# Optimization experiments

Measured on AMD Instinct MI355X. Metric: run time of the kernel, lower is better.

Reference implementation:

```python
import jax, jax.numpy as jnp
import numpy as np

N, E, G = 51200, 819200, 256            # nodes, directed edges, graphs
N2, A, E2 = 102400, 204800, 409600      # 2-sets, assignments, 2-set edges
D, L, NI2, NAF = 64, 5, 36, 40          # emb_dim, num_layer, num_i_2, num_atom_features
EPS = 1e-5


def _seg_sum(v, seg, n):
    return jax.ops.segment_sum(v, seg, num_segments=n)


def _seg_mean(v, seg, n):
    s = jax.ops.segment_sum(v, seg, num_segments=n)
    c = jax.ops.segment_sum(jnp.ones((v.shape[0],), v.dtype), seg, num_segments=n)
    return s / jnp.maximum(c, 1.0)[:, None]


def setup_inputs() -> dict:
    key = jax.random.key(0)
    ks = iter(jax.random.split(key, 64))
    nrm = lambda shape: jax.random.normal(next(ks), shape, jnp.float32) * 0.1
    x = jax.random.normal(next(ks), (N, NAF), jnp.float32)
    edge_index = jax.random.randint(next(ks), (2, E), 0, N, dtype=jnp.int32)
    edge_attr = jnp.stack([jax.random.randint(next(ks), (E,), 0, 4, dtype=jnp.int32),
                           jax.random.randint(next(ks), (E,), 0, 3, dtype=jnp.int32)], axis=1)
    batch = jnp.repeat(jnp.arange(G, dtype=jnp.int32), N // G)
    iso_type_2 = jax.nn.one_hot(jax.random.randint(next(ks), (N2,), 0, NI2), NI2, dtype=jnp.float32)
    edge_index_2 = jax.random.randint(next(ks), (2, E2), 0, N2, dtype=jnp.int32)
    assignment_index_2 = jnp.stack([jax.random.randint(next(ks), (A,), 0, N, dtype=jnp.int32),
                                    jnp.repeat(jnp.arange(N2, dtype=jnp.int32), 2)], axis=0)
    batch_2 = jnp.repeat(jnp.arange(G, dtype=jnp.int32), N2 // G)
    params = dict(
        emb_W=nrm((NAF, D)), emb_b=jnp.zeros((D,), jnp.float32),
        gin_W1=nrm((L, D, 2 * D)), gin_b1=jnp.zeros((L, 2 * D), jnp.float32),
        gin_W2=nrm((L, 2 * D, D)), gin_b2=jnp.zeros((L, D), jnp.float32),
        eemb1=nrm((L, 6, D)), eemb2=nrm((L, 3, D)),
        bn_gamma=jnp.ones((L, D), jnp.float32), bn_beta=jnp.zeros((L, D), jnp.float32),
        iso1_rel_W=nrm((D + NI2, D)), iso1_rel_b=jnp.zeros((D,), jnp.float32),
        iso1_root_W=nrm((D + NI2, D)),
        iso2_rel_W=nrm((D, D)), iso2_rel_b=jnp.zeros((D,), jnp.float32),
        iso2_root_W=nrm((D, D)),
        ro_W0=nrm((2 * D, D)), ro_b0=jnp.zeros((D,), jnp.float32),
        ro_W1=nrm((D, D // 2)), ro_b1=jnp.zeros((D // 2,), jnp.float32),
        ro_W2=nrm((D // 2, D // 4)), ro_b2=jnp.zeros((D // 4,), jnp.float32),
        last_W=nrm((D // 4, 1)), last_b=jnp.zeros((1,), jnp.float32),
    )
    return dict(x=x, edge_index=edge_index, edge_attr=edge_attr, batch=batch,
                iso_type_2=iso_type_2, edge_index_2=edge_index_2,
                assignment_index_2=assignment_index_2, batch_2=batch_2, **params)


def _forward(x, iso_type_2, emb_W, emb_b, gin_W1, gin_b1, gin_W2, gin_b2,
             eemb1, eemb2, bn_gamma, bn_beta,
             iso1_rel_W, iso1_rel_b, iso1_root_W, iso2_rel_W, iso2_rel_b, iso2_root_W,
             ro_W0, ro_b0, ro_W1, ro_b1, ro_W2, ro_b2, last_W, last_b,
             edge_index, edge_attr, batch, edge_index_2, assignment_index_2, batch_2):
    # --- GIN stack with edge-feature embeddings and self loops ---
    loop = jnp.arange(N, dtype=edge_index.dtype)
    src = jnp.concatenate([edge_index[0], loop])
    dst = jnp.concatenate([edge_index[1], loop])
    sl_attr = jnp.tile(jnp.array([[4, 0]], dtype=edge_attr.dtype), (N, 1))
    ea = jnp.concatenate([edge_attr, sl_attr], axis=0)  # [E+N, 2]

    h = jax.nn.relu(x @ emb_W + emb_b)  # x_embedding1
    for l in range(L):
        e = eemb1[l][ea[:, 0]] + eemb2[l][ea[:, 1]]      # [E+N, D]
        agg = _seg_sum(h[src] + e, dst, N)               # gather + scatter-add
        h2 = jax.nn.relu(agg @ gin_W1[l] + gin_b1[l]) @ gin_W2[l] + gin_b2[l]
        mu = jnp.mean(h2, axis=0)
        var = jnp.var(h2, axis=0)                        # biased, torch BN training mode
        h2 = (h2 - mu) / jnp.sqrt(var + EPS) * bn_gamma[l] + bn_beta[l]
        h = h2 if l == L - 1 else jax.nn.relu(h2)        # last layer: no ReLU (JK='last')
    node_rep = h

    # --- graph mean pool of node representation ---
    x1 = _seg_mean(node_rep, batch, G)                   # [G, D]

    # --- 2-set branch: avg_pool onto 2-sets, concat iso type, two GraphConvs ---
    xp = _seg_mean(node_rep[assignment_index_2[0]], assignment_index_2[1], N2)
    xp = jnp.concatenate([xp, iso_type_2], axis=1)       # [N2, D+NI2]

    def graph_conv(z, Wrel, brel, Wroot):
        agg = _seg_sum(z[edge_index_2[0]], edge_index_2[1], N2)
        return agg @ Wrel + brel + z @ Wroot

    xp = jax.nn.relu(graph_conv(xp, iso1_rel_W, iso1_rel_b, iso1_root_W))
    xp = jax.nn.relu(graph_conv(xp, iso2_rel_W, iso2_rel_b, iso2_root_W))
    x2 = _seg_mean(xp, batch_2, G)                       # [G, D]

    # --- readout MLP ---
    m = jnp.concatenate([x1, x2], axis=1)                # [G, 2D]
    m = jax.nn.relu(m @ ro_W0 + ro_b0)
    m = jax.nn.relu(m @ ro_W1 + ro_b1)
    m = jax.nn.relu(m @ ro_W2 + ro_b2)
    m = m @ last_W + last_b
    return m.reshape(-1)                                 # num_tasks == 1 -> flat [G]


def reference(x, edge_index, edge_attr, batch, iso_type_2, edge_index_2,
              assignment_index_2, batch_2, emb_W, emb_b, gin_W1, gin_b1, gin_W2,
              gin_b2, eemb1, eemb2, bn_gamma, bn_beta, iso1_rel_W, iso1_rel_b,
              iso1_root_W, iso2_rel_W, iso2_rel_b, iso2_root_W, ro_W0, ro_b0,
              ro_W1, ro_b1, ro_W2, ro_b2, last_W, last_b):
    return _forward(x, iso_type_2, emb_W, emb_b, gin_W1, gin_b1, gin_W2, gin_b2,
                    eemb1, eemb2, bn_gamma, bn_beta,
                    iso1_rel_W, iso1_rel_b, iso1_root_W, iso2_rel_W, iso2_rel_b,
                    iso2_root_W, ro_W0, ro_b0, ro_W1, ro_b1, ro_W2, ro_b2,
                    last_W, last_b, edge_index, edge_attr, batch, edge_index_2,
                    assignment_index_2, batch_2)
```

## Files before the change

kernel.cpp:

```cpp
#include <hip/hip_runtime.h>

#define NN   51200
#define EE   819200
#define GG   256
#define NN2  102400
#define AA   204800
#define EE2  409600
#define DD   64
#define LL   5

#define NB1  100
#define NB2  200
#define CAP1 10240
#define CAP2 3072

typedef __attribute__((ext_vector_type(8))) short bf16x8;
typedef __attribute__((ext_vector_type(4))) float f32x4;
typedef unsigned short ushort_t;

#define OFF_H      ((size_t)0)
#define OFF_AGG    ((size_t)13107200)
#define OFF_H2     ((size_t)26214400)
#define OFF_XP     ((size_t)39321600)
#define OFF_REC1   OFF_XP
// ... 110 lines not shown
    int v = (tid < nb) ? cnt[tid] : 0;
    int incl = waveInclScan(v, lane);
    if (lane == 63) wsum[wid] = incl;
    __syncthreads();
    int woff = 0;
#pragma unroll
    for (int w = 0; w < 3; ++w) woff += (w < wid) ? wsum[w] : 0;
    if (tid < nb) base[tid] = woff + incl - v;
}

__global__ __launch_bounds__(256) void kbB(const int* __restrict__ bucketCnt,
                                           const int* __restrict__ bucketBase,
                                           const int2* __restrict__ rec1, const int2* __restrict__ rec2,
                                           int* __restrict__ offs1, int* __restrict__ col1,
                                           int* __restrict__ offs2, int* __restrict__ col2,
                                           int* __restrict__ dbin) {
    __shared__ int nh[512];
    __shared__ int ncur[512];
    __shared__ int wsum[4];
    __shared__ int dhist[64];
    int tid = threadIdx.x, b = blockIdx.x;
    bool g1 = b < NB1;
    const int2* rec = g1 ? (rec1 + (size_t)b * CAP1) : (rec2 + (size_t)(b - NB1) * CAP2);
    int cnt = bucketCnt[b];
    int base = bucketBase[b];
    int* offs = g1 ? offs1 : offs2;
    int* col = g1 ? col1 : col2;
    int nodeBase = g1 ? b * 512 : (b - NB1) * 512;
    nh[tid] = 0; nh[tid + 256] = 0;
    if (tid < 64) dhist[tid] = 0;
    __syncthreads();
    for (int e = tid; e < cnt; e += 256) {
        int2 r = rec[e];
        atomicAdd(&nh[r.y & 511], 1);
    }
    __syncthreads();
    int v0 = nh[2 * tid], v1 = nh[2 * tid + 1];
    int s = v0 + v1;
    int lane = tid & 63, wid = tid >> 6;
    int incl = waveInclScan(s, lane);
    if (lane == 63) wsum[wid] = incl;
    __syncthreads();
    int woff = 0;
#pragma unroll
    for (int w = 0; w < 3; ++w) woff += (w < wid) ? wsum[w] : 0;
    int excl = woff + incl - s;
    ncur[2 * tid] = excl;
    ncur[2 * tid + 1] = excl + v0;
    offs[nodeBase + 2 * tid] = base + excl;
    offs[nodeBase + 2 * tid + 1] = base + excl + v0;
    if (g1) {
        atomicAdd(&dhist[v0 < 63 ? v0 : 63], 1);
        atomicAdd(&dhist[v1 < 63 ? v1 : 63], 1);
    }
    __syncthreads();
    for (int e = tid; e < cnt; e += 256) {
        int2 r = rec[e];
        int node = r.y & 511;
        int slot = base + atomicAdd(&ncur[node], 1);
        col[slot] = r.x;
    }
    if (g1 && tid < 64 && dhist[tid]) atomicAdd(&dbin[tid], dhist[tid]);
    if (tid == 0) {
        if (b == NB1 - 1) offs1[NN] = EE;
        if (b == NB1 + NB2 - 1) offs2[NN2] = EE2;
    }
}

__global__ __launch_bounds__(256) void kiso(const float* __restrict__ iso, int* __restrict__ isoIdx) {
    __shared__ float srow[256 * 36];
    int tid = threadIdx.x;
    int base = blockIdx.x * 256;
    const float4* g4p = (const float4*)(iso + (size_t)base * 36);
#pragma unroll
    for (int i = tid; i < 2304; i += 256) ((float4*)srow)[i] = g4p[i];
    __syncthreads();
    const float* r = srow + tid * 36;
    int best = 0;
#pragma unroll
    for (int k = 0; k < 36; ++k)
        if (r[k] > 0.5f) best = k;
    isoIdx[base + tid] = best;
}

__global__ void kprepx(const float* __restrict__ x, const float* __restrict__ embW,
                       const float* __restrict__ embB, float* __restrict__ h,
                       const float* __restrict__ gW1, const float* __restrict__ gW2,
                       ushort_t* __restrict__ w1h, ushort_t* __restrict__ w1l,
                       ushort_t* __restrict__ w2h, ushort_t* __restrict__ w2l,
                       const float* __restrict__ i1rW, const float* __restrict__ i1tW,
                       const float* __restrict__ i2rW, const float* __restrict__ i2tW,
                       ushort_t* __restrict__ gcwh, ushort_t* __restrict__ gcwl) {
    int b = blockIdx.x;
    if (b < 12800) {
        int t = b * 256 + threadIdx.x;
        int n = t >> 6, d = t & 63;
        float acc = embB[d];
        const float4* xr4 = (const float4*)(x + (size_t)n * 40);
#pragma unroll
        for (int k4 = 0; k4 < 10; ++k4) {
            float4 xv = xr4[k4];
            acc = fmaf(xv.x, embW[(4 * k4 + 0) * 64 + d], acc);
            acc = fmaf(xv.y, embW[(4 * k4 + 1) * 64 + d], acc);
            acc = fmaf(xv.z, embW[(4 * k4 + 2) * 64 + d], acc);
            acc = fmaf(xv.w, embW[(4 * k4 + 3) * 64 + d], acc);
        }
        h[(size_t)n * 64 + d] = fmaxf(acc, 0.f);
    } else if (b < 12840) {
        int t = (b - 12800) * 256 + threadIdx.x;
        int lane = t & 63, frag = t >> 6;
        int c15 = lane & 15, q = lane >> 4;
        if (frag < 80) {
            int kt = frag & 1, nt = (frag >> 1) & 7, l = frag >> 4;
            const float* W = gW1 + l * 8192;
            ushort_t* oh = w1h + ((size_t)frag * 64 + lane) * 8;
            ushort_t* ol = w1l + ((size_t)frag * 64 + lane) * 8;
            int kb = kt * 32 + q * 8, colw = nt * 16 + c15;
#pragma unroll
            for (int j = 0; j < 8; ++j) {
                ushort_t hi, lo; bsplit(W[(kb + j) * 128 + colw], hi, lo);
                oh[j] = hi; ol[j] = lo;
            }
        } else if (frag < 160) {
            int f = frag - 80;
            int kt = f & 3, nt = (f >> 2) & 3, l = f >> 4;
            const float* W = gW2 + l * 8192;
            ushort_t* oh = w2h + ((size_t)f * 64 + lane) * 8;
            ushort_t* ol = w2l + ((size_t)f * 64 + lane) * 8;
            int kb = kt * 32 + q * 8, colw = nt * 16 + c15;
#pragma unroll
            for (int j = 0; j < 8; ++j) {
                ushort_t hi, lo; bsplit(W[(kb + j) * 64 + colw], hi, lo);
                oh[j] = hi; ol[j] = lo;
            }
        }
    } else {
        int t = (b - 12840) * 256 + threadIdx.x;
        int lane = t & 63, frag = t >> 6;
        int c15 = lane & 15, q = lane >> 4;
        int m = frag >> 3, f = frag & 7;
        int kt = f & 1, nt = f >> 1;
        const float* W = (m == 0) ? i1rW : (m == 1) ? i1tW : (m == 2) ? i2rW : i2tW;
        ushort_t* oh = gcwh + (size_t)m * 4096 + ((size_t)f * 64 + lane) * 8;
        ushort_t* ol = gcwl + (size_t)m * 4096 + ((size_t)f * 64 + lane) * 8;
        int kb = kt * 32 + q * 8, colw = nt * 16 + c15;
#pragma unroll
        for (int j = 0; j < 8; ++j) {
            ushort_t hi, lo; bsplit(W[(kb + j) * 64 + colw], hi, lo);
            oh[j] = hi; ol[j] = lo;
        }
    }
}

__global__ void kdegscan(const int* __restrict__ dbin, int* __restrict__ dstart) {
    int tid = threadIdx.x;
    int v = dbin[tid];
    int incl = waveInclScan(v, tid);
    dstart[tid] = incl - v;
}

__global__ __launch_bounds__(256) void kdegplace(const int* __restrict__ offs,
                                                 const int* __restrict__ dstart,
                                                 int* __restrict__ dcur,
                                                 int* __restrict__ perm) {
    __shared__ int lhist[64];
    __shared__ int lbase[64];
    int tid = threadIdx.x;
    if (tid < 64) lhist[tid] = 0;
    __syncthreads();
    int n = blockIdx.x * 256 + tid;
    int d = offs[n + 1] - offs[n]; d = d < 63 ? d : 63;
    int lr = atomicAdd(&lhist[d], 1);
    __syncthreads();
    if (tid < 64) {
        int c = lhist[tid];
        lbase[tid] = c ? atomicAdd(&dcur[tid], c) : 0;
    }
    __syncthreads();
    perm[dstart[d] + lbase[d] + lr] = n;
}

__global__ __launch_bounds__(256) void ktrans(float* __restrict__ h,
                                              const float* __restrict__ pst,
                                              const float* __restrict__ gamma,
                                              const float* __restrict__ beta) {
    __shared__ float sstat[128];
    __shared__ float sSC[64], sSH[64];
    int tid = threadIdx.x;
    if (tid < 128) {
        float s = 0.f;
        const float* p = pst + tid;
#pragma unroll
        for (int i = 0; i < 32; ++i) s += p[i * 128];
        sstat[tid] = s;
    }
    __syncthreads();
    if (tid < 64) {
        float mu = sstat[tid] * (1.f / NN);
        float var = sstat[64 + tid] * (1.f / NN) - mu * mu;
        float sc = gamma[tid] * rsqrtf(var + 1e-5f);
        sSC[tid] = sc; sSH[tid] = beta[tid] - mu * sc;
    }
    __syncthreads();
    int c = (tid & 15) * 4;
    float4 sc4 = *(const float4*)(sSC + c);
    float4 sh4 = *(const float4*)(sSH + c);
    float4* hp = (float4*)h;
    size_t base = (size_t)blockIdx.x * 1024 + tid;
#pragma unroll
    for (int r = 0; r < 4; ++r) {
        float4 v = hp[base + r * 256];
        v.x = fmaxf(fmaf(v.x, sc4.x, sh4.x), 0.f);
        v.y = fmaxf(fmaf(v.y, sc4.y, sh4.y), 0.f);
        v.z = fmaxf(fmaf(v.z, sc4.z, sh4.z), 0.f);
        v.w = fmaxf(fmaf(v.w, sc4.w, sh4.w), 0.f);
        hp[base + r * 256] = v;
    }
}

__global__ __launch_bounds__(256) void kglayer(
    const float* __restrict__ hin, float* __restrict__ hout,
    const int* __restrict__ perm,
    const int* __restrict__ offs, const int* __restrict__ col,
    const float* __restrict__ e1, const float* __restrict__ e2,
    const ushort_t* __restrict__ w1h, const ushort_t* __restrict__ w1l,
    const ushort_t* __restrict__ w2h, const ushort_t* __restrict__ w2l,
    const float* __restrict__ b1, const float* __restrict__ b2,
    float* __restrict__ pstout) {
    __shared__ float etab[13 * 64];
    __shared__ int sPerm[16];
    __shared__ float sMLP[16 * 132];
    float* sA = sMLP;
    float* sH = sMLP;
    int tid = threadIdx.x;
    if (tid < 16) sPerm[tid] = perm[blockIdx.x * 16 + tid];
    for (int idx = tid; idx < 13 * 64; idx += 256) {
        int ci = idx >> 6, dd = idx & 63;
        etab[idx] = e1[(ci / 3) * 64 + dd] + e2[(ci % 3) * 64 + dd];
    }
    __syncthreads();
    int lane = tid & 63, wv = tid >> 6;
    int c15 = lane & 15, q = lane >> 4;

    {
        int n = sPerm[wv * 4 + q];
        int s0 = offs[n], s1 = offs[n + 1];
        float4 sx = *(const float4*)(hin + (size_t)n * 64 + 4 * c15);
        float4 et = *(const float4*)(etab + 12 * 64 + 4 * c15);
        float a0 = sx.x + et.x, a1 = sx.y + et.y, a2 = sx.z + et.z, a3 = sx.w + et.w;
        int deg = s1 - s0;
        if (deg > 0) {
            const int* cp = col + s0;
            int nfull = deg >> 3, rem = deg & 7;
            int vv[8];
#pragma unroll
            for (int j = 0; j < 8; ++j) {
                int idx = j < deg ? j : deg - 1;
                vv[j] = cp[idx];
            }
            for (int it = 0; it < nfull; ++it) {
                float4 xv[8], tv[8];
#pragma unroll
                for (int j = 0; j < 8; ++j) {
                    xv[j] = *(const float4*)(hin + (size_t)(vv[j] & 0xFFFF) * 64 + 4 * c15);
                    tv[j] = *(const float4*)(etab + (vv[j] >> 16) * 64 + 4 * c15);
                }
                int e8 = (it + 1) * 8;
                bool more = e8 < deg;
                int nx[8];
                if (more) {
#pragma unroll
                    for (int j = 0; j < 8; ++j) {
                        int idx = e8 + j; idx = idx < deg ? idx : deg - 1;
                        nx[j] = cp[idx];
                    }
                }
#pragma unroll
                for (int j = 0; j < 8; ++j) {
                    a0 += xv[j].x + tv[j].x;
                    a1 += xv[j].y + tv[j].y;
                    a2 += xv[j].z + tv[j].z;
                    a3 += xv[j].w + tv[j].w;
                }
                if (more) {
#pragma unroll
                    for (int j = 0; j < 8; ++j) vv[j] = nx[j];
                }
            }
            if (rem) {
                float4 xv[8], tv[8];
#pragma unroll
                for (int j = 0; j < 8; ++j) {
                    xv[j] = *(const float4*)(hin + (size_t)(vv[j] & 0xFFFF) * 64 + 4 * c15);
                    tv[j] = *(const float4*)(etab + (vv[j] >> 16) * 64 + 4 * c15);
                }
#pragma unroll
                for (int j = 0; j < 8; ++j) {
                    float mm = (j < rem) ? 1.f : 0.f;
                    a0 = fmaf(xv[j].x + tv[j].x, mm, a0);
                    a1 = fmaf(xv[j].y + tv[j].y, mm, a1);
                    a2 = fmaf(xv[j].z + tv[j].z, mm, a2);
                    a3 = fmaf(xv[j].w + tv[j].w, mm, a3);
                }
            }
        }
        *(float4*)(sA + (wv * 4 + q) * 68 + 4 * c15) = make_float4(a0, a1, a2, a3);
    }
    __syncthreads();

    bf16x8 ah[2], al[2];
#pragma unroll
    for (int kt = 0; kt < 2; ++kt) {
        const float* p = sA + c15 * 68 + kt * 32 + q * 8;
        float4 x0 = *(const float4*)p;
        float4 x1 = *(const float4*)(p + 4);
        float xs[8] = {x0.x, x0.y, x0.z, x0.w, x1.x, x1.y, x1.z, x1.w};
#pragma unroll
        for (int j = 0; j < 8; ++j) {
            ushort_t hi, lo; bsplit(xs[j], hi, lo);
            ah[kt][j] = (short)hi; al[kt][j] = (short)lo;
        }
    }
    __syncthreads();

    f32x4 acc1[2];
#pragma unroll
    for (int j = 0; j < 2; ++j) { f32x4 z = {0.f, 0.f, 0.f, 0.f}; acc1[j] = z; }
#pragma unroll
    for (int kt = 0; kt < 2; ++kt) {
#pragma unroll
        for (int j = 0; j < 2; ++j) {
            int nt = 2 * wv + j;
            size_t fo = ((size_t)((nt * 2 + kt) * 64 + lane)) * 8;
            bf16x8 bh = *(const bf16x8*)(w1h + fo);
            bf16x8 bl = *(const bf16x8*)(w1l + fo);
            acc1[j] = __builtin_amdgcn_mfma_f32_16x16x32_bf16(ah[kt], bh, acc1[j], 0, 0, 0);
            acc1[j] = __builtin_amdgcn_mfma_f32_16x16x32_bf16(al[kt], bh, acc1[j], 0, 0, 0);
            acc1[j] = __builtin_amdgcn_mfma_f32_16x16x32_bf16(ah[kt], bl, acc1[j], 0, 0, 0);
        }
    }
#pragma unroll
    for (int j = 0; j < 2; ++j) {
        int nt = 2 * wv + j;
        float bias = b1[nt * 16 + c15];
#pragma unroll
        for (int rg = 0; rg < 4; ++rg)
            sH[(4 * q + rg) * 132 + nt * 16 + c15] = fmaxf(acc1[j][rg] + bias, 0.f);
    }
    __syncthreads();

    f32x4 acc2 = {0.f, 0.f, 0.f, 0.f};
#pragma unroll
    for (int kt = 0; kt < 4; ++kt) {
        const float* p = sH + c15 * 132 + kt * 32 + q * 8;
        float4 x0 = *(const float4*)p;
        float4 x1 = *(const float4*)(p + 4);
        float xs[8] = {x0.x, x0.y, x0.z, x0.w, x1.x, x1.y, x1.z, x1.w};
        bf16x8 a2h, a2l;
#pragma unroll
        for (int j = 0; j < 8; ++j) {
            ushort_t hi, lo; bsplit(xs[j], hi, lo);
            a2h[j] = (short)hi; a2l[j] = (short)lo;
        }
        size_t fo = ((size_t)((wv * 4 + kt) * 64 + lane)) * 8;
        bf16x8 bh = *(const bf16x8*)(w2h + fo);
        bf16x8 bl = *(const bf16x8*)(w2l + fo);
        acc2 = __builtin_amdgcn_mfma_f32_16x16x32_bf16(a2h, bh, acc2, 0, 0, 0);
        acc2 = __builtin_amdgcn_mfma_f32_16x16x32_bf16(a2l, bh, acc2, 0, 0, 0);
        acc2 = __builtin_amdgcn_mfma_f32_16x16x32_bf16(a2h, bl, acc2, 0, 0, 0);
    }
    {
        float bias = b2[wv * 16 + c15];
        float s = 0.f, s2 = 0.f;
#pragma unroll
        for (int rg = 0; rg < 4; ++rg) {
            float v = acc2[rg] + bias;
            hout[(size_t)sPerm[4 * q + rg] * 64 + wv * 16 + c15] = v;
            s += v; s2 += v * v;
        }
        s += __shfl_xor(s, 16, 64);  s += __shfl_xor(s, 32, 64);
        s2 += __shfl_xor(s2, 16, 64); s2 += __shfl_xor(s2, 32, 64);
        if (q == 0) {
            float* ps = pstout + (size_t)(blockIdx.x & 31) * 128;
            atomicAdd(&ps[wv * 16 + c15], s);
            atomicAdd(&ps[64 + wv * 16 + c15], s2);
        }
    }
}

template <int FIRST>
__global__ __launch_bounds__(256) void kgcmm(const float* __restrict__ X,
                                             const ushort_t* __restrict__ grh,
                                             const ushort_t* __restrict__ grl,
                                             const ushort_t* __restrict__ gth,
                                             const ushort_t* __restrict__ gtl,
                                             const float* __restrict__ WrelIso,
                                             const float* __restrict__ WrootIso,
                                             const int* __restrict__ isoIdx,
                                             float* __restrict__ Yrel,
                                             float* __restrict__ Yroot,
                                             const float* __restrict__ pst,
                                             const float* __restrict__ g4,
                                             const float* __restrict__ b4,
                                             const int* __restrict__ a0g,
                                             const float* __restrict__ h2src) {
    __shared__ float sX[64 * 68];
    __shared__ float sstat[128];
    __shared__ float sSC[64], sSH[64];
    int tid = threadIdx.x, blk = blockIdx.x;
    if (FIRST && tid < 128) {
        float s = 0.f;
        const float* p = pst + tid;
#pragma unroll
        for (int i = 0; i < 32; ++i) s += p[i * 128];
        sstat[tid] = s;
    }
    __syncthreads();
    if (FIRST && tid < 64) {
        float mu = sstat[tid] * (1.f / NN);
        float var = sstat[64 + tid] * (1.f / NN) - mu * mu;
        float sc = g4[tid] * rsqrtf(var + 1e-5f);
        sSC[tid] = sc;
        sSH[tid] = b4[tid] - mu * sc;
    }
    __syncthreads();
#pragma unroll
    for (int i = tid; i < 1024; i += 256) {
        int row = i >> 4, c = (i & 15) << 2;
        float4 v;
        if (FIRST) {
            int grow = blk * 64 + row;
            int na = a0g[2 * grow], nb = a0g[2 * grow + 1];
            float4 va = *(const float4*)(h2src + (size_t)na * 64 + c);
            float4 vb = *(const float4*)(h2src + (size_t)nb * 64 + c);
            v.x = 0.5f * (va.x + vb.x); v.y = 0.5f * (va.y + vb.y);
            v.z = 0.5f * (va.z + vb.z); v.w = 0.5f * (va.w + vb.w);
            v.x = fmaf(v.x, sSC[c], sSH[c]);
            v.y = fmaf(v.y, sSC[c + 1], sSH[c + 1]);
            v.z = fmaf(v.z, sSC[c + 2], sSH[c + 2]);
            v.w = fmaf(v.w, sSC[c + 3], sSH[c + 3]);
        } else {
            v = ((const float4*)(X + (size_t)blk * 4096))[i];
        }
        float* p = sX + row * 68 + c;
        p[0] = v.x; p[1] = v.y; p[2] = v.z; p[3] = v.w;
    }
    __syncthreads();
    int lane = tid & 63, wv = tid >> 6;
    int c15 = lane & 15, q = lane >> 4;

    bf16x8 ah[2], al[2];
#pragma unroll
    for (int kt = 0; kt < 2; ++kt) {
        const float* p = sX + (16 * wv + c15) * 68 + kt * 32 + q * 8;
        float4 x0 = *(const float4*)p;
        float4 x1 = *(const float4*)(p + 4);
        float xs[8] = {x0.x, x0.y, x0.z, x0.w, x1.x, x1.y, x1.z, x1.w};
#pragma unroll
        for (int j = 0; j < 8; ++j) {
            ushort_t hi, lo; bsplit(xs[j], hi, lo);
            ah[kt][j] = (short)hi; al[kt][j] = (short)lo;
        }
    }

    f32x4 accR[4], accT[4];
#pragma unroll
    for (int nt = 0; nt < 4; ++nt) {
        f32x4 z = {0.f, 0.f, 0.f, 0.f};
        accR[nt] = z; accT[nt] = z;
    }
#pragma unroll
    for (int nt = 0; nt < 4; ++nt) {
#pragma unroll
        for (int kt = 0; kt < 2; ++kt) {
            size_t fo = ((size_t)((nt * 2 + kt) * 64 + lane)) * 8;
            bf16x8 bh = *(const bf16x8*)(grh + fo);
            bf16x8 bl = *(const bf16x8*)(grl + fo);
            accR[nt] = __builtin_amdgcn_mfma_f32_16x16x32_bf16(ah[kt], bh, accR[nt], 0, 0, 0);
            accR[nt] = __builtin_amdgcn_mfma_f32_16x16x32_bf16(al[kt], bh, accR[nt], 0, 0, 0);
            accR[nt] = __builtin_amdgcn_mfma_f32_16x16x32_bf16(ah[kt], bl, accR[nt], 0, 0, 0);
            bf16x8 ch = *(const bf16x8*)(gth + fo);
            bf16x8 cl = *(const bf16x8*)(gtl + fo);
            accT[nt] = __builtin_amdgcn_mfma_f32_16x16x32_bf16(ah[kt], ch, accT[nt], 0, 0, 0);
            accT[nt] = __builtin_amdgcn_mfma_f32_16x16x32_bf16(al[kt], ch, accT[nt], 0, 0, 0);
            accT[nt] = __builtin_amdgcn_mfma_f32_16x16x32_bf16(ah[kt], cl, accT[nt], 0, 0, 0);
        }
    }

    int rbase = blk * 64 + 16 * wv + 4 * q;
#pragma unroll
    for (int rg = 0; rg < 4; ++rg) {
        int row = rbase + rg;
        int ii = FIRST ? isoIdx[row] : 0;
        float* yr = Yrel + (size_t)row * 64;
        float* yt = Yroot + (size_t)row * 64;
        const float* er = WrelIso + (size_t)ii * 64;
        const float* et = WrootIso + (size_t)ii * 64;
#pragma unroll
        for (int nt = 0; nt < 4; ++nt) {
            int cc = nt * 16 + c15;
            float vr = accR[nt][rg], vt = accT[nt][rg];
            if (FIRST) { vr += er[cc]; vt += et[cc]; }
            yr[cc] = vr;
            yt[cc] = vt;
        }
    }
}

__global__ void kgather2(const float* __restrict__ yrel, const float* __restrict__ yroot,
                         const float* __restrict__ brel, const int* __restrict__ offs,
                         const int* __restrict__ col, float* __restrict__ out) {
    int t = blockIdx.x * 256 + threadIdx.x;
    int j = t >> 4, c = t & 15;
    int s0 = offs[j], s1 = offs[j + 1];
    float4 rt = *(const float4*)(yroot + (size_t)j * 64 + 4 * c);
    float4 bb = *(const float4*)(brel + 4 * c);
    float a0 = rt.x + bb.x, a1 = rt.y + bb.y, a2 = rt.z + bb.z, a3 = rt.w + bb.w;
    if (s0 < s1) {
        int vv[4];
#pragma unroll
        for (int jj = 0; jj < 4; ++jj) {
            int idx = s0 + jj; idx = idx < s1 ? idx : s1 - 1;
            vv[jj] = col[idx];
        }
        int e = s0;
        while (true) {
            int ne = e + 4;
            bool more = ne < s1;
            float4 xs[4];
#pragma unroll
            for (int jj = 0; jj < 4; ++jj)
                xs[jj] = *(const float4*)(yrel + (size_t)vv[jj] * 64 + 4 * c);
            int nx[4];
            if (more) {
#pragma unroll
                for (int jj = 0; jj < 4; ++jj) {
                    int idx = ne + jj; idx = idx < s1 ? idx : s1 - 1;
                    nx[jj] = col[idx];
                }
            }
#pragma unroll
            for (int jj = 0; jj < 4; ++jj) {
                float mm = (e + jj < s1) ? 1.f : 0.f;
                a0 = fmaf(xs[jj].x, mm, a0);
                a1 = fmaf(xs[jj].y, mm, a1);
                a2 = fmaf(xs[jj].z, mm, a2);
                a3 = fmaf(xs[jj].w, mm, a3);
            }
            if (!more) break;
            e = ne;
#pragma unroll
            for (int jj = 0; jj < 4; ++jj) vv[jj] = nx[jj];
        }
    }
    *(float4*)(out + (size_t)j * 64 + 4 * c) =
        make_float4(fmaxf(a0, 0.f), fmaxf(a1, 0.f), fmaxf(a2, 0.f), fmaxf(a3, 0.f));
}

__global__ void kpoolg(const float* __restrict__ h2, const float* __restrict__ xp2,
                       const float* __restrict__ pst, const float* __restrict__ g4,
                       const float* __restrict__ b4, float* __restrict__ m) {
    __shared__ float sstat[128];
    __shared__ float red[4][64];
    int g = blockIdx.x, tid = threadIdx.x;
    if (tid < 128) {
        float s = 0.f;
        const float* p = pst + tid;
#pragma unroll
        for (int i = 0; i < 32; ++i) s += p[i * 128];
        sstat[tid] = s;
    }
    int wid = tid >> 6, d = tid & 63;
    float s1 = 0.f;
    for (int i = wid; i < 200; i += 4) s1 += h2[((size_t)g * 200 + i) * 64 + d];
    red[wid][d] = s1;
    __syncthreads();
    if (wid == 0) {
        float mean = (red[0][d] + red[1][d] + red[2][d] + red[3][d]) * (1.f / 200.f);
        float mu = sstat[d] * (1.f / NN);
        float var = sstat[64 + d] * (1.f / NN) - mu * mu;
        float sc = g4[d] * rsqrtf(var + 1e-5f);
        m[g * 128 + d] = fmaf(mean, sc, b4[d] - mu * sc);
    }
    __syncthreads();
    float s2 = 0.f;
    for (int i = wid; i < 400; i += 4) s2 += xp2[((size_t)g * 400 + i) * 64 + d];
    red[wid][d] = s2;
    __syncthreads();
    if (wid == 0) m[g * 128 + 64 + d] = (red[0][d] + red[1][d] + red[2][d] + red[3][d]) * (1.f / 400.f);
}

__global__ void kread(const float* __restrict__ m, const float* __restrict__ W0,
                      const float* __restrict__ b0, const float* __restrict__ W1,
                      const float* __restrict__ b1, const float* __restrict__ W2,
                      const float* __restrict__ b2, const float* __restrict__ lw,
                      const float* __restrict__ lb, float* __restrict__ out) {
    __shared__ float s0[64], s1[32], s2[16];
    int g = blockIdx.x, d = threadIdx.x;
    const float* mr = m + g * 128;
    float t = b0[d];
    for (int k = 0; k < 128; ++k) t = fmaf(mr[k], W0[k * 64 + d], t);
    s0[d] = fmaxf(t, 0.f);
    __syncthreads();
    if (d < 32) {
        float u = b1[d];
        for (int k = 0; k < 64; ++k) u = fmaf(s0[k], W1[k * 32 + d], u);
        s1[d] = fmaxf(u, 0.f);
    }
    __syncthreads();
    if (d < 16) {
        float u = b2[d];
        for (int k = 0; k < 32; ++k) u = fmaf(s1[k], W2[k * 16 + d], u);
        s2[d] = fmaxf(u, 0.f);
    }
    __syncthreads();
    if (d == 0) {
        float u = lb[0];
        for (int k = 0; k < 16; ++k) u = fmaf(s2[k], lw[k], u);
        out[g] = u;
    }
}

extern "C" void kernel_launch(void* const* d_in, const int* in_sizes, int n_in,
                              void* d_out, int out_size, void* d_ws, size_t ws_size,
                              hipStream_t stream) {
    if (ws_size < WS_NEEDED) return;

    const float* x    = (const float*)d_in[0];
    const int*   ei   = (const int*)d_in[1];
    const int*   ea   = (const int*)d_in[2];
    const float* iso  = (const float*)d_in[4];
    const int*   ei2  = (const int*)d_in[5];
    const int*   ai2  = (const int*)d_in[6];
    const float* embW = (const float*)d_in[8];
    const float* embB = (const float*)d_in[9];
    const float* gW1  = (const float*)d_in[10];
    const float* gB1  = (const float*)d_in[11];
    const float* gW2  = (const float*)d_in[12];
    const float* gB2  = (const float*)d_in[13];
    const float* ee1  = (const float*)d_in[14];
    const float* ee2  = (const float*)d_in[15];
    const float* bng  = (const float*)d_in[16];
    const float* bnb  = (const float*)d_in[17];
    const float* i1rW = (const float*)d_in[18];
    const float* i1rB = (const float*)d_in[19];
    const float* i1tW = (const float*)d_in[20];
    const float* i2rW = (const float*)d_in[21];
    const float* i2rB = (const float*)d_in[22];
    const float* i2tW = (const float*)d_in[23];
    const float* roW0 = (const float*)d_in[24];
    const float* roB0 = (const float*)d_in[25];
    const float* roW1 = (const float*)d_in[26];
    const float* roB1 = (const float*)d_in[27];
    const float* roW2 = (const float*)d_in[28];
    const float* roB2 = (const float*)d_in[29];
    const float* lW   = (const float*)d_in[30];
    const float* lB   = (const float*)d_in[31];
    float* out = (float*)d_out;

    char* ws = (char*)d_ws;
    float* h      = (float*)(ws + OFF_H);
    float* hB     = (float*)(ws + OFF_AGG);
    float* hA     = (float*)(ws + OFF_H2);
    float* h2     = hA;
    float* xp     = (float*)(ws + OFF_XP);
    float* yrel   = (float*)(ws + OFF_H);
    float* yroot  = (float*)(ws + OFF_YROOT);
    int* offs1    = (int*)(ws + OFF_OFFS1);
    int* col1     = (int*)(ws + OFF_COL1);
    int* offs2    = (int*)(ws + OFF_OFFS2);
    int* col2     = (int*)(ws + OFF_COL2);
    int* isoIdx   = (int*)(ws + OFF_ISO);
    float* mbuf   = (float*)(ws + OFF_M);
    ushort_t* w1h = (ushort_t*)(ws + OFF_YROOT);
    ushort_t* w1l = (ushort_t*)(ws + OFF_YROOT + 81920);
    ushort_t* w2h = (ushort_t*)(ws + OFF_YROOT + 163840);
    ushort_t* w2l = (ushort_t*)(ws + OFF_YROOT + 245760);
    ushort_t* gcwh = (ushort_t*)(ws + OFF_M);
    ushort_t* gcwl = (ushort_t*)(ws + OFF_M + 32768);
    float* pstat2 = (float*)(ws + OFF_CUR1);
    int2* rec1    = (int2*)(ws + OFF_REC1);
    int2* rec2    = (int2*)(ws + OFF_REC2);
    int* bucketCnt  = (int*)(ws + OFF_CNT1);
    int* bucketBase = (int*)(ws + OFF_BBASE);
    int* perm     = (int*)(ws + OFF_PERM);
    int* dbin     = (int*)(ws + OFF_STATS);
    int* dstart   = dbin + 64;
    int* dcur     = dbin + 128;

    const int* src1 = ei;
    const int* dst1 = ei + EE;
    const int* src2 = ei2;
    const int* dst2 = ei2 + EE2;
    const int* a0   = ai2;

    hipMemsetAsync(ws + OFF_CNT1, 0, ZERO_BYTES, stream);

    kbA<<<600, 256, 0, stream>>>(src1, dst1, ea, src2, dst2, bucketCnt, rec1, rec2);
    kiso<<<NN2 / 256, 256, 0, stream>>>(iso, isoIdx);
    kprepx<<<12848, 256, 0, stream>>>(x, embW, embB, h, gW1, gW2,
                                      w1h, w1l, w2h, w2l,
                                      i1rW, i1tW, i2rW, i2tW, gcwh, gcwl);
    kbscan<<<2, 256, 0, stream>>>(bucketCnt, bucketBase);
    kbB<<<300, 256, 0, stream>>>(bucketCnt, bucketBase, rec1, rec2,
                                 offs1, col1, offs2, col2, dbin);
    kdegscan<<<1, 64, 0, stream>>>(dbin, dstart);
    kdegplace<<<NN / 256, 256, 0, stream>>>(offs1, dstart, dcur, perm);

    for (int l = 0; l < LL; ++l) {
        const float* hin = (l == 0) ? h : ((l & 1) ? hA : hB);
        float* hout = (l & 1) ? hB : hA;
        kglayer<<<NN / 16, 256, 0, stream>>>(
            hin, hout, perm, offs1, col1, ee1 + l * 384, ee2 + l * 192,
            w1h + (size_t)l * 8192, w1l + (size_t)l * 8192,
            w2h + (size_t)l * 8192, w2l + (size_t)l * 8192,
            gB1 + l * 128, gB2 + l * 64,
            pstat2 + (size_t)l * 4096);
        if (l < LL - 1)
            ktrans<<<800, 256, 0, stream>>>(hout, pstat2 + (size_t)l * 4096,
                                            bng + l * 64, bnb + l * 64);
    }

    kgcmm<1><<<NN2 / 64, 256, 0, stream>>>(xp,
                                           gcwh, gcwl, gcwh + 4096, gcwl + 4096,
                                           i1rW + 64 * 64, i1tW + 64 * 64, isoIdx,
                                           yrel, yroot,
                                           pstat2 + (size_t)4 * 4096,
                                           bng + 4 * 64, bnb + 4 * 64, a0, h2);
    kgather2<<<NN2 * 16 / 256, 256, 0, stream>>>(yrel, yroot, i1rB, offs2, col2, xp);
    kgcmm<0><<<NN2 / 64, 256, 0, stream>>>(xp,
                                           gcwh + 8192, gcwl + 8192, gcwh + 12288, gcwl + 12288,
                                           nullptr, nullptr, nullptr,
                                           yrel, yroot,
                                           nullptr, nullptr, nullptr, nullptr, nullptr);
    kgather2<<<NN2 * 16 / 256, 256, 0, stream>>>(yrel, yroot, i2rB, offs2, col2, xp);

    kpoolg<<<GG, 256, 0, stream>>>(h2, xp, pstat2 + (size_t)4 * 4096,
                                   bng + 4 * 64, bnb + 4 * 64, mbuf);
    kread<<<GG, 64, 0, stream>>>(mbuf, roW0, roB0, roW1, roB1, roW2, roB2, lW, lB, out);
}
```

Baseline: 572.1 us.

## Fold batchnorm into next GIN layer, merge degree scan, aggregate-then-transform for conv2

Removes the separate ktrans pass by applying the previous layer's batchnorm and ReLU on the fly inside the next kglayer's gather, and folds the degree-bin scan into kdegplace. For the second graph conv it switches from transform-then-gather to gather-then-transform: first sum the raw neighbour features, then a fused dual GEMM applies the rel and root weights with bias and ReLU. This cuts kernel launches and full-tensor read/write passes. In exchange, every gathered neighbour now pays an extra fma and max per element, and each block recomputes the BN statistics.

```diff
diff --git a/kernel.cpp b/kernel.cpp
--- a/kernel.cpp
+++ b/kernel.cpp
@@ -286,21 +286,20 @@
     }
 }
 
-__global__ void kdegscan(const int* __restrict__ dbin, int* __restrict__ dstart) {
-    int tid = threadIdx.x;
-    int v = dbin[tid];
-    int incl = waveInclScan(v, tid);
-    dstart[tid] = incl - v;
-}
-
 __global__ __launch_bounds__(256) void kdegplace(const int* __restrict__ offs,
-                                                 const int* __restrict__ dstart,
+                                                 const int* __restrict__ dbin,
                                                  int* __restrict__ dcur,
                                                  int* __restrict__ perm) {
     __shared__ int lhist[64];
     __shared__ int lbase[64];
+    __shared__ int sdstart[64];
     int tid = threadIdx.x;
-    if (tid < 64) lhist[tid] = 0;
+    if (tid < 64) {
+        lhist[tid] = 0;
+        int v = dbin[tid];
+        int incl = waveInclScan(v, tid);
+        sdstart[tid] = incl - v;
+    }
     __syncthreads();
     int n = blockIdx.x * 256 + tid;
     int d = offs[n + 1] - offs[n]; d = d < 63 ? d : 63;
@@ -311,47 +310,10 @@
         lbase[tid] = c ? atomicAdd(&dcur[tid], c) : 0;
     }
     __syncthreads();
-    perm[dstart[d] + lbase[d] + lr] = n;
-}
-
-__global__ __launch_bounds__(256) void ktrans(float* __restrict__ h,
-                                              const float* __restrict__ pst,
-                                              const float* __restrict__ gamma,
-                                              const float* __restrict__ beta) {
-    __shared__ float sstat[128];
-    __shared__ float sSC[64], sSH[64];
-    int tid = threadIdx.x;
-    if (tid < 128) {
-        float s = 0.f;
-        const float* p = pst + tid;
-#pragma unroll
-        for (int i = 0; i < 32; ++i) s += p[i * 128];
-        sstat[tid] = s;
-    }
-    __syncthreads();
-    if (tid < 64) {
-        float mu = sstat[tid] * (1.f / NN);
-        float var = sstat[64 + tid] * (1.f / NN) - mu * mu;
-        float sc = gamma[tid] * rsqrtf(var + 1e-5f);
-        sSC[tid] = sc; sSH[tid] = beta[tid] - mu * sc;
-    }
-    __syncthreads();
-    int c = (tid & 15) * 4;
-    float4 sc4 = *(const float4*)(sSC + c);
-    float4 sh4 = *(const float4*)(sSH + c);
-    float4* hp = (float4*)h;
-    size_t base = (size_t)blockIdx.x * 1024 + tid;
-#pragma unroll
-    for (int r = 0; r < 4; ++r) {
-        float4 v = hp[base + r * 256];
-        v.x = fmaxf(fmaf(v.x, sc4.x, sh4.x), 0.f);
-        v.y = fmaxf(fmaf(v.y, sc4.y, sh4.y), 0.f);
-        v.z = fmaxf(fmaf(v.z, sc4.z, sh4.z), 0.f);
-        v.w = fmaxf(fmaf(v.w, sc4.w, sh4.w), 0.f);
-        hp[base + r * 256] = v;
-    }
-}
-
+    perm[sdstart[d] + lbase[d] + lr] = n;
+}
+
+template <int FOLD_BN>
 __global__ __launch_bounds__(256) void kglayer(
     const float* __restrict__ hin, float* __restrict__ hout,
     const int* __restrict__ perm,
@@ -360,9 +322,11 @@
     const ushort_t* __restrict__ w1h, const ushort_t* __restrict__ w1l,
     const ushort_t* __restrict__ w2h, const ushort_t* __restrict__ w2l,
     const float* __restrict__ b1, const float* __restrict__ b2,
-    float* __restrict__ pstout) {
+    const float* __restrict__ pst, const float* __restrict__ gamma,
+    const float* __restrict__ beta, float* __restrict__ pstout) {
     __shared__ float etab[13 * 64];
     __shared__ int sPerm[16];
+    __shared__ float sstat[128];
     __shared__ float sMLP[16 * 132];
     float* sA = sMLP;
     float* sH = sMLP;
@@ -372,16 +336,43 @@
         int ci = idx >> 6, dd = idx & 63;
         etab[idx] = e1[(ci / 3) * 64 + dd] + e2[(ci % 3) * 64 + dd];
     }
+    if (FOLD_BN && tid < 128) {
+        float s = 0.f;
+        const float* p = pst + tid;
+#pragma unroll
+        for (int i = 0; i < 32; ++i) s += p[i * 128];
+        sstat[tid] = s;
+    }
     __syncthreads();
     int lane = tid & 63, wv = tid >> 6;
     int c15 = lane & 15, q = lane >> 4;
+
+    float sc0 = 1.f, sc1 = 1.f, sc2 = 1.f, sc3 = 1.f;
+    float sh0 = 0.f, sh1 = 0.f, sh2 = 0.f, sh3 = 0.f;
+    if (FOLD_BN) {
+        int ch = 4 * c15;
+        float mu, var;
+        mu = sstat[ch] * (1.f / NN); var = sstat[64 + ch] * (1.f / NN) - mu * mu;
+        sc0 = gamma[ch] * rsqrtf(var + 1e-5f); sh0 = beta[ch] - mu * sc0;
+        mu = sstat[ch + 1] * (1.f / NN); var = sstat[65 + ch] * (1.f / NN) - mu * mu;
+        sc1 = gamma[ch + 1] * rsqrtf(var + 1e-5f); sh1 = beta[ch + 1] - mu * sc1;
+        mu = sstat[ch + 2] * (1.f / NN); var = sstat[66 + ch] * (1.f / NN) - mu * mu;
+        sc2 = gamma[ch + 2] * rsqrtf(var + 1e-5f); sh2 = beta[ch + 2] - mu * sc2;
+        mu = sstat[ch + 3] * (1.f / NN); var = sstat[67 + ch] * (1.f / NN) - mu * mu;
+        sc3 = gamma[ch + 3] * rsqrtf(var + 1e-5f); sh3 = beta[ch + 3] - mu * sc3;
+    }
 
     {
         int n = sPerm[wv * 4 + q];
         int s0 = offs[n], s1 = offs[n + 1];
         float4 sx = *(const float4*)(hin + (size_t)n * 64 + 4 * c15);
         float4 et = *(const float4*)(etab + 12 * 64 + 4 * c15);
-        float a0 = sx.x + et.x, a1 = sx.y + et.y, a2 = sx.z + et.z, a3 = sx.w + et.w;
+        float x0 = sx.x, x1 = sx.y, x2 = sx.z, x3 = sx.w;
+        if (FOLD_BN) {
+            x0 = fmaxf(fmaf(x0, sc0, sh0), 0.f); x1 = fmaxf(fmaf(x1, sc1, sh1), 0.f);
+            x2 = fmaxf(fmaf(x2, sc2, sh2), 0.f); x3 = fmaxf(fmaf(x3, sc3, sh3), 0.f);
+        }
+        float a0 = x0 + et.x, a1 = x1 + et.y, a2 = x2 + et.z, a3 = x3 + et.w;
         int deg = s1 - s0;
         if (deg > 0) {
             const int* cp = col + s0;
@@ -411,10 +402,17 @@
                 }
 #pragma unroll
                 for (int j = 0; j < 8; ++j) {
-                    a0 += xv[j].x + tv[j].x;
-                    a1 += xv[j].y + tv[j].y;
-                    a2 += xv[j].z + tv[j].z;
-                    a3 += xv[j].w + tv[j].w;
+                    float y0 = xv[j].x, y1 = xv[j].y, y2 = xv[j].z, y3 = xv[j].w;
+                    if (FOLD_BN) {
+                        y0 = fmaxf(fmaf(y0, sc0, sh0), 0.f);
+                        y1 = fmaxf(fmaf(y1, sc1, sh1), 0.f);
+                        y2 = fmaxf(fmaf(y2, sc2, sh2), 0.f);
+                        y3 = fmaxf(fmaf(y3, sc3, sh3), 0.f);
+                    }
+                    a0 += y0 + tv[j].x;
+                    a1 += y1 + tv[j].y;
+                    a2 += y2 + tv[j].z;
+                    a3 += y3 + tv[j].w;
                 }
                 if (more) {
 #pragma unroll
@@ -431,10 +429,17 @@
 #pragma unroll
                 for (int j = 0; j < 8; ++j) {
                     float mm = (j < rem) ? 1.f : 0.f;
-                    a0 = fmaf(xv[j].x + tv[j].x, mm, a0);
-                    a1 = fmaf(xv[j].y + tv[j].y, mm, a1);
-                    a2 = fmaf(xv[j].z + tv[j].z, mm, a2);
-                    a3 = fmaf(xv[j].w + tv[j].w, mm, a3);
+                    float y0 = xv[j].x, y1 = xv[j].y, y2 = xv[j].z, y3 = xv[j].w;
+                    if (FOLD_BN) {
+                        y0 = fmaxf(fmaf(y0, sc0, sh0), 0.f);
+                        y1 = fmaxf(fmaf(y1, sc1, sh1), 0.f);
+                        y2 = fmaxf(fmaf(y2, sc2, sh2), 0.f);
+                        y3 = fmaxf(fmaf(y3, sc3, sh3), 0.f);
+                    }
+                    a0 = fmaf(y0 + tv[j].x, mm, a0);
+                    a1 = fmaf(y1 + tv[j].y, mm, a1);
+                    a2 = fmaf(y2 + tv[j].z, mm, a2);
+                    a3 = fmaf(y3 + tv[j].w, mm, a3);
                 }
             }
         }
@@ -522,27 +527,25 @@
     }
 }
 
-template <int FIRST>
-__global__ __launch_bounds__(256) void kgcmm(const float* __restrict__ X,
-                                             const ushort_t* __restrict__ grh,
-                                             const ushort_t* __restrict__ grl,
-                                             const ushort_t* __restrict__ gth,
-                                             const ushort_t* __restrict__ gtl,
-                                             const float* __restrict__ WrelIso,
-                                             const float* __restrict__ WrootIso,
-                                             const int* __restrict__ isoIdx,
-                                             float* __restrict__ Yrel,
-                                             float* __restrict__ Yroot,
-                                             const float* __restrict__ pst,
-                                             const float* __restrict__ g4,
-                                             const float* __restrict__ b4,
-                                             const int* __restrict__ a0g,
-                                             const float* __restrict__ h2src) {
+__global__ __launch_bounds__(256) void kgcmm1(const ushort_t* __restrict__ grh,
+                                              const ushort_t* __restrict__ grl,
+                                              const ushort_t* __restrict__ gth,
+                                              const ushort_t* __restrict__ gtl,
+                                              const float* __restrict__ WrelIso,
+                                              const float* __restrict__ WrootIso,
+                                              const int* __restrict__ isoIdx,
+                                              float* __restrict__ Yrel,
+                                              float* __restrict__ Yroot,
+                                              const float* __restrict__ pst,
+                                              const float* __restrict__ g4,
+                                              const float* __restrict__ b4,
+                                              const int* __restrict__ a0g,
+                                              const float* __restrict__ h2src) {
     __shared__ float sX[64 * 68];
     __shared__ float sstat[128];
     __shared__ float sSC[64], sSH[64];
     int tid = threadIdx.x, blk = blockIdx.x;
-    if (FIRST && tid < 128) {
+    if (tid < 128) {
         float s = 0.f;
         const float* p = pst + tid;
 #pragma unroll
@@ -550,7 +553,7 @@
         sstat[tid] = s;
     }
     __syncthreads();
-    if (FIRST && tid < 64) {
+    if (tid < 64) {
         float mu = sstat[tid] * (1.f / NN);
         float var = sstat[64 + tid] * (1.f / NN) - mu * mu;
         float sc = g4[tid] * rsqrtf(var + 1e-5f);
@@ -561,21 +564,17 @@
 #pragma unroll
     for (int i = tid; i < 1024; i += 256) {
         int row = i >> 4, c = (i & 15) << 2;
+        int grow = blk * 64 + row;
+        int na = a0g[2 * grow], nb = a0g[2 * grow + 1];
+        float4 va = *(const float4*)(h2src + (size_t)na * 64 + c);
+        float4 vb = *(const float4*)(h2src + (size_t)nb * 64 + c);
         float4 v;
-        if (FIRST) {
-            int grow = blk * 64 + row;
-            int na = a0g[2 * grow], nb = a0g[2 * grow + 1];
-            float4 va = *(const float4*)(h2src + (size_t)na * 64 + c);
-            float4 vb = *(const float4*)(h2src + (size_t)nb * 64 + c);
-            v.x = 0.5f * (va.x + vb.x); v.y = 0.5f * (va.y + vb.y);
-            v.z = 0.5f * (va.z + vb.z); v.w = 0.5f * (va.w + vb.w);
-            v.x = fmaf(v.x, sSC[c], sSH[c]);
-            v.y = fmaf(v.y, sSC[c + 1], sSH[c + 1]);
-            v.z = fmaf(v.z, sSC[c + 2], sSH[c + 2]);
-            v.w = fmaf(v.w, sSC[c + 3], sSH[c + 3]);
-        } else {
-            v = ((const float4*)(X + (size_t)blk * 4096))[i];
-        }
+        v.x = 0.5f * (va.x + vb.x); v.y = 0.5f * (va.y + vb.y);
+        v.z = 0.5f * (va.z + vb.z); v.w = 0.5f * (va.w + vb.w);
+        v.x = fmaf(v.x, sSC[c], sSH[c]);
+        v.y = fmaf(v.y, sSC[c + 1], sSH[c + 1]);
+        v.z = fmaf(v.z, sSC[c + 2], sSH[c + 2]);
+        v.w = fmaf(v.w, sSC[c + 3], sSH[c + 3]);
         float* p = sX + row * 68 + c;
         p[0] = v.x; p[1] = v.y; p[2] = v.z; p[3] = v.w;
     }
@@ -625,7 +624,7 @@
 #pragma unroll
     for (int rg = 0; rg < 4; ++rg) {
         int row = rbase + rg;
-        int ii = FIRST ? isoIdx[row] : 0;
+        int ii = isoIdx[row];
         float* yr = Yrel + (size_t)row * 64;
         float* yt = Yroot + (size_t)row * 64;
         const float* er = WrelIso + (size_t)ii * 64;
@@ -633,10 +632,86 @@
 #pragma unroll
         for (int nt = 0; nt < 4; ++nt) {
             int cc = nt * 16 + c15;
-            float vr = accR[nt][rg], vt = accT[nt][rg];
-            if (FIRST) { vr += er[cc]; vt += et[cc]; }
-            yr[cc] = vr;
-            yt[cc] = vt;
+            yr[cc] = accR[nt][rg] + er[cc];
+            yt[cc] = accT[nt][rg] + et[cc];
+        }
+    }
+}
+
+__global__ __launch_bounds__(256) void kgcmm2(const float* __restrict__ AGG,
+                                              const float* __restrict__ XP,
+                                              const ushort_t* __restrict__ grh,
+                                              const ushort_t* __restrict__ grl,
+                                              const ushort_t* __restrict__ gth,
+                                              const ushort_t* __restrict__ gtl,
+                                              const float* __restrict__ brel,
+                                              float* __restrict__ OUT) {
+    __shared__ float sA[64 * 68];
+    __shared__ float sB[64 * 68];
+    int tid = threadIdx.x, blk = blockIdx.x;
+#pragma unroll
+    for (int i = tid; i < 1024; i += 256) {
+        int row = i >> 4, c = (i & 15) << 2;
+        float4 va = ((const float4*)(AGG + (size_t)blk * 4096))[i];
+        float4 vb = ((const float4*)(XP + (size_t)blk * 4096))[i];
+        float* pa = sA + row * 68 + c;
+        float* pb = sB + row * 68 + c;
+        pa[0] = va.x; pa[1] = va.y; pa[2] = va.z; pa[3] = va.w;
+        pb[0] = vb.x; pb[1] = vb.y; pb[2] = vb.z; pb[3] = vb.w;
+    }
+    __syncthreads();
+    int lane = tid & 63, wv = tid >> 6;
+    int c15 = lane & 15, q = lane >> 4;
+
+    bf16x8 aAh[2], aAl[2], aBh[2], aBl[2];
+#pragma unroll
+    for (int kt = 0; kt < 2; ++kt) {
+        const float* pa = sA + (16 * wv + c15) * 68 + kt * 32 + q * 8;
+        const float* pb = sB + (16 * wv + c15) * 68 + kt * 32 + q * 8;
+        float4 a0 = *(const float4*)pa;
+        float4 a1 = *(const float4*)(pa + 4);
+        float4 b0 = *(const float4*)pb;
+        float4 b1 = *(const float4*)(pb + 4);
+        float as[8] = {a0.x, a0.y, a0.z, a0.w, a1.x, a1.y, a1.z, a1.w};
+        float bs[8] = {b0.x, b0.y, b0.z, b0.w, b1.x, b1.y, b1.z, b1.w};
+#pragma unroll
+        for (int j = 0; j < 8; ++j) {
+            ushort_t hi, lo;
+            bsplit(as[j], hi, lo); aAh[kt][j] = (short)hi; aAl[kt][j] = (short)lo;
+            bsplit(bs[j], hi, lo); aBh[kt][j] = (short)hi; aBl[kt][j] = (short)lo;
+        }
+    }
+
+    f32x4 acc[4];
+#pragma unroll
+    for (int nt = 0; nt < 4; ++nt) { f32x4 z = {0.f, 0.f, 0.f, 0.f}; acc[nt] = z; }
+#pragma unroll
+    for (int nt = 0; nt < 4; ++nt) {
+#pragma unroll
+        for (int kt = 0; kt < 2; ++kt) {
+            size_t fo = ((size_t)((nt * 2 + kt) * 64 + lane)) * 8;
+            bf16x8 bh = *(const bf16x8*)(grh + fo);
+            bf16x8 bl = *(const bf16x8*)(grl + fo);
+            acc[nt] = __builtin_amdgcn_mfma_f32_16x16x32_bf16(aAh[kt], bh, acc[nt], 0, 0, 0);
+            acc[nt] = __builtin_amdgcn_mfma_f32_16x16x32_bf16(aAl[kt], bh, acc[nt], 0, 0, 0);
+            acc[nt] = __builtin_amdgcn_mfma_f32_16x16x32_bf16(aAh[kt], bl, acc[nt], 0, 0, 0);
+            bf16x8 ch = *(const bf16x8*)(gth + fo);
+            bf16x8 cl = *(const bf16x8*)(gtl + fo);
+            acc[nt] = __builtin_amdgcn_mfma_f32_16x16x32_bf16(aBh[kt], ch, acc[nt], 0, 0, 0);
+            acc[nt] = __builtin_amdgcn_mfma_f32_16x16x32_bf16(aBl[kt], ch, acc[nt], 0, 0, 0);
+            acc[nt] = __builtin_amdgcn_mfma_f32_16x16x32_bf16(aBh[kt], cl, acc[nt], 0, 0, 0);
+        }
+    }
+
+    int rbase = blk * 64 + 16 * wv + 4 * q;
+#pragma unroll
+    for (int rg = 0; rg < 4; ++rg) {
+        int row = rbase + rg;
+        float* yo = OUT + (size_t)row * 64;
+#pragma unroll
+        for (int nt = 0; nt < 4; ++nt) {
+            int cc = nt * 16 + c15;
+            yo[cc] = fmaxf(acc[nt][rg] + brel[cc], 0.f);
         }
     }
 }
@@ -689,6 +764,52 @@
     }
     *(float4*)(out + (size_t)j * 64 + 4 * c) =
         make_float4(fmaxf(a0, 0.f), fmaxf(a1, 0.f), fmaxf(a2, 0.f), fmaxf(a3, 0.f));
+}
+
+__global__ void kgather2raw(const float* __restrict__ xpsrc, const int* __restrict__ offs,
+                            const int* __restrict__ col, float* __restrict__ agg) {
+    int t = blockIdx.x * 256 + threadIdx.x;
+    int j = t >> 4, c = t & 15;
+    int s0 = offs[j], s1 = offs[j + 1];
+    float a0 = 0.f, a1 = 0.f, a2 = 0.f, a3 = 0.f;
+    if (s0 < s1) {
+        int vv[4];
+#pragma unroll
+        for (int jj = 0; jj < 4; ++jj) {
+            int idx = s0 + jj; idx = idx < s1 ? idx : s1 - 1;
+            vv[jj] = col[idx];
+        }
+        int e = s0;
+        while (true) {
+            int ne = e + 4;
+            bool more = ne < s1;
+            float4 xs[4];
+#pragma unroll
+            for (int jj = 0; jj < 4; ++jj)
+                xs[jj] = *(const float4*)(xpsrc + (size_t)vv[jj] * 64 + 4 * c);
+            int nx[4];
+            if (more) {
+#pragma unroll
+                for (int jj = 0; jj < 4; ++jj) {
+                    int idx = ne + jj; idx = idx < s1 ? idx : s1 - 1;
+                    nx[jj] = col[idx];
+                }
+            }
+#pragma unroll
+            for (int jj = 0; jj < 4; ++jj) {
+                float mm = (e + jj < s1) ? 1.f : 0.f;
+                a0 = fmaf(xs[jj].x, mm, a0);
+                a1 = fmaf(xs[jj].y, mm, a1);
+                a2 = fmaf(xs[jj].z, mm, a2);
+                a3 = fmaf(xs[jj].w, mm, a3);
+            }
+            if (!more) break;
+            e = ne;
+#pragma unroll
+            for (int jj = 0; jj < 4; ++jj) vv[jj] = nx[jj];
+        }
+    }
+    *(float4*)(agg + (size_t)j * 64 + 4 * c) = make_float4(a0, a1, a2, a3);
 }
 
 __global__ void kpoolg(const float* __restrict__ h2, const float* __restrict__ xp2,
@@ -800,6 +921,8 @@
     float* xp     = (float*)(ws + OFF_XP);
     float* yrel   = (float*)(ws + OFF_H);
     float* yroot  = (float*)(ws + OFF_YROOT);
+    float* aggb   = (float*)(ws + OFF_H);
+    float* xp2    = (float*)(ws + OFF_YROOT);
     int* offs1    = (int*)(ws + OFF_OFFS1);
     int* col1     = (int*)(ws + OFF_COL1);
     int* offs2    = (int*)(ws + OFF_OFFS2);
@@ -819,8 +942,7 @@
     int* bucketBase = (int*)(ws + OFF_BBASE);
     int* perm     = (int*)(ws + OFF_PERM);
     int* dbin     = (int*)(ws + OFF_STATS);
-    int* dstart   = dbin + 64;
-    int* dcur     = dbin + 128;
+    int* dcur     = dbin + 64;
 
     const int* src1 = ei;
     const int* dst1 = ei + EE;
@@ -838,38 +960,40 @@
     kbscan<<<2, 256, 0, stream>>>(bucketCnt, bucketBase);
     kbB<<<300, 256, 0, stream>>>(bucketCnt, bucketBase, rec1, rec2,
                                  offs1, col1, offs2, col2, dbin);
-    kdegscan<<<1, 64, 0, stream>>>(dbin, dstart);
-    kdegplace<<<NN / 256, 256, 0, stream>>>(offs1, dstart, dcur, perm);
+    kdegplace<<<NN / 256, 256, 0, stream>>>(offs1, dbin, dcur, perm);
 
     for (int l = 0; l < LL; ++l) {
         const float* hin = (l == 0) ? h : ((l & 1) ? hA : hB);
         float* hout = (l & 1) ? hB : hA;
-        kglayer<<<NN / 16, 256, 0, stream>>>(
-            hin, hout, perm, offs1, col1, ee1 + l * 384, ee2 + l * 192,
-            w1h + (size_t)l * 8192, w1l + (size_t)l * 8192,
-            w2h + (size_t)l * 8192, w2l + (size_t)l * 8192,
-            gB1 + l * 128, gB2 + l * 64,
-            pstat2 + (size_t)l * 4096);
-        if (l < LL - 1)
-            ktrans<<<800, 256, 0, stream>>>(hout, pstat2 + (size_t)l * 4096,
-                                            bng + l * 64, bnb + l * 64);
-    }
-
-    kgcmm<1><<<NN2 / 64, 256, 0, stream>>>(xp,
-                                           gcwh, gcwl, gcwh + 4096, gcwl + 4096,
-                                           i1rW + 64 * 64, i1tW + 64 * 64, isoIdx,
-                                           yrel, yroot,
-                                           pstat2 + (size_t)4 * 4096,
-                                           bng + 4 * 64, bnb + 4 * 64, a0, h2);
+        if (l == 0) {
+            kglayer<0><<<NN / 16, 256, 0, stream>>>(
+                hin, hout, perm, offs1, col1, ee1, ee2,
+                w1h, w1l, w2h, w2l, gB1, gB2,
+                nullptr, nullptr, nullptr, pstat2);
+        } else {
+            kglayer<1><<<NN / 16, 256, 0, stream>>>(
+                hin, hout, perm, offs1, col1, ee1 + l * 384, ee2 + l * 192,
+                w1h + (size_t)l * 8192, w1l + (size_t)l * 8192,
+                w2h + (size_t)l * 8192, w2l + (size_t)l * 8192,
+                gB1 + l * 128, gB2 + l * 64,
+                pstat2 + (size_t)(l - 1) * 4096,
+                bng + (l - 1) * 64, bnb + (l - 1) * 64,
+                pstat2 + (size_t)l * 4096);
+        }
+    }
+
+    kgcmm1<<<NN2 / 64, 256, 0, stream>>>(gcwh, gcwl, gcwh + 4096, gcwl + 4096,
+                                         i1rW + 64 * 64, i1tW + 64 * 64, isoIdx,
+                                         yrel, yroot,
+                                         pstat2 + (size_t)4 * 4096,
+                                         bng + 4 * 64, bnb + 4 * 64, a0, h2);
     kgather2<<<NN2 * 16 / 256, 256, 0, stream>>>(yrel, yroot, i1rB, offs2, col2, xp);
-    kgcmm<0><<<NN2 / 64, 256, 0, stream>>>(xp,
-                                           gcwh + 8192, gcwl + 8192, gcwh + 12288, gcwl + 12288,
-                                           nullptr, nullptr, nullptr,
-                                           yrel, yroot,
-                                           nullptr, nullptr, nullptr, nullptr, nullptr);
-    kgather2<<<NN2 * 16 / 256, 256, 0, stream>>>(yrel, yroot, i2rB, offs2, col2, xp);
-
-    kpoolg<<<GG, 256, 0, stream>>>(h2, xp, pstat2 + (size_t)4 * 4096,
+    kgather2raw<<<NN2 * 16 / 256, 256, 0, stream>>>(xp, offs2, col2, aggb);
+    kgcmm2<<<NN2 / 64, 256, 0, stream>>>(aggb, xp,
+                                         gcwh + 8192, gcwl + 8192, gcwh + 12288, gcwl + 12288,
+                                         i2rB, xp2);
+
+    kpoolg<<<GG, 256, 0, stream>>>(h2, xp2, pstat2 + (size_t)4 * 4096,
                                    bng + 4 * 64, bnb + 4 * 64, mbuf);
     kread<<<GG, 64, 0, stream>>>(mbuf, roW0, roB0, roW1, roB1, roW2, roB2, lW, lB, out);
 }
```

After: 598.7 us. +4.6%, slower.
